# Performance work log

Measured on AMD Instinct MI355X. Metric: run time of the kernel, lower is better.

The kernel has to match this reference:

```python
import jax, jax.numpy as jnp
import numpy as np

B, H, KVH, D = 32, 32, 8, 128          # batch, q heads, kv heads, head_size
S = 2048                                # context length per sequence
BLOCK_SIZE = 16                         # tokens per cache block
NUM_BLOCKS = B * (S // BLOCK_SIZE)      # 4096
BASE = 10000.0
SCALE = 1.0 / D ** 0.5


def setup_inputs() -> dict:
    key = jax.random.key(0)
    kq, kk, kv = jax.random.split(key, 3)
    query = jax.random.normal(kq, (B, H, D), dtype=jnp.float32)
    # paged KV cache: [num_blocks, block_size * kv_heads * head_size]
    k_cache = jax.random.normal(kk, (NUM_BLOCKS, BLOCK_SIZE * KVH * D), dtype=jnp.float32)
    v_cache = jax.random.normal(kv, (NUM_BLOCKS, BLOCK_SIZE * KVH * D), dtype=jnp.float32)
    # contiguous slot layout: slot[i, p] = i * S + p  (>=0 means valid)
    slot_mapping = jnp.arange(B * S, dtype=jnp.int32).reshape(B, S)
    # per-sequence token positions 0..S-1
    positions = jnp.broadcast_to(jnp.arange(S, dtype=jnp.int32), (B, S))
    return {"query": query, "k_cache": k_cache, "v_cache": v_cache,
            "slot_mapping": slot_mapping, "positions": positions}


def _rope(x, pos):
    """x: [B, h, s, D], pos: [B, s] int -> rotary-embedded x (RotaryEmbedding.forward)."""
    inv_freq = 1.0 / (BASE ** (jnp.arange(0, D, 2, dtype=jnp.float32) / D))   # [D/2]
    freqs = pos[..., None].astype(jnp.float32) * inv_freq                     # [B, s, D/2]
    emb = jnp.concatenate([freqs, freqs], axis=-1)                            # [B, s, D]
    cos = jnp.cos(emb)[:, None]                                               # [B, 1, s, D]
    sin = jnp.sin(emb)[:, None]
    x1, x2 = x[..., : D // 2], x[..., D // 2 :]
    rotated = jnp.concatenate([-x2, x1], axis=-1)
    return x * cos + rotated * sin


def reference(query, k_cache, v_cache, slot_mapping, positions):
    # --- paged gather (the per-slot loop in _compatible_forward, vectorized) ---
    valid = slot_mapping >= 0                                  # [B, S]
    slots = jnp.where(valid, slot_mapping, 0)
    blk = slots // BLOCK_SIZE
    off = slots % BLOCK_SIZE
    kc = k_cache.reshape(NUM_BLOCKS, BLOCK_SIZE, KVH, D)
    vc = v_cache.reshape(NUM_BLOCKS, BLOCK_SIZE, KVH, D)
    k = kc[blk, off]                                           # [B, S, KVH, D]
    v = vc[blk, off]
    m = valid[..., None, None]
    k = jnp.where(m, k, 0.0).transpose(0, 2, 1, 3)             # [B, KVH, S, D]
    v = jnp.where(m, v, 0.0).transpose(0, 2, 1, 3)

    # --- rotary: q at its (last) position, keys at all cached positions ---
    q = query[:, :, None, :]                                   # [B, H, 1, D]
    q = _rope(q, positions[:, -1:])
    k = _rope(k, positions)

    # --- GQA: repeat_interleave kv heads to match q heads ---
    rep = H // KVH
    k = jnp.repeat(k, rep, axis=1)                             # [B, H, S, D]
    v = jnp.repeat(v, rep, axis=1)

    scores = jnp.einsum('bhqd,bhkd->bhqk', q, k) * SCALE       # [B, H, 1, S]
    weights = jax.nn.softmax(scores, axis=-1)
    out = jnp.einsum('bhqk,bhkd->bhqd', weights, v)            # [B, H, 1, D]
    return out[:, :, 0, :]                                     # [B, H, D]
```

## Files before the change

kernel.cpp:

```cpp
#include <hip/hip_runtime.h>
#include <math.h>

#define B_    32
#define H_    32
#define KVH_  8
#define D_    128
#define S_    2048
#define REP   4
#define PAIRS 256
#define SCALE 0.08838834764831845f

typedef unsigned int u32;

__device__ __forceinline__ void dma16(const float* g, float* l) {
    __builtin_amdgcn_global_load_lds(
        (const __attribute__((address_space(1))) u32*)g,
        (__attribute__((address_space(3))) u32*)l,
        16, 0, 0);
}

#define WAITVM(N) asm volatile("s_waitcnt vmcnt(" #N ")" ::: "memory")

__global__ __launch_bounds__(64) void rope_q(
    const float* __restrict__ query,
    const int*   __restrict__ positions,
    float* __restrict__ q_rot,
    float* __restrict__ invf_tab)
{
    const int head = blockIdx.x;
    const int b    = head >> 5;
    const int j    = threadIdx.x;
    const double invf = exp(-(double)j * (9.210340371976184 / 64.0));
    if (head == 0) invf_tab[j] = (float)invf;
    const int posq = positions[b * S_ + (S_ - 1)];
    const double fr = (double)posq * invf;
    const float cs = (float)cos(fr), sn = (float)sin(fr);
    const float* q = query + (size_t)head * D_;
    const float lo = q[j], hi = q[64 + j];
    float* o = q_rot + (size_t)head * D_;
    o[j]      = (lo * cs - hi * sn) * SCALE;
    o[64 + j] = (hi * cs + lo * sn) * SCALE;
}

extern __shared__ char smem_raw[];

__global__ __launch_bounds__(128, 4) void pa_main(
    const float* __restrict__ query,
    const float* __restrict__ k_cache,
    const float* __restrict__ v_cache,
    const int*   __restrict__ slot_map,
    const int*   __restrict__ positions,
    const float* __restrict__ q_rot,
    const float* __restrict__ invf_tab,
    float* __restrict__ ws_l,
    float* __restrict__ ws_acc,
    float* __restrict__ out,
    int cpp, int wpb, int use_qrot)
{
    const int w     = threadIdx.x >> 6;
    const int ln    = threadIdx.x & 63;
    const int g     = ln & 15;
    const int ts    = ln >> 4;
    const int chunk = S_ / cpp;
    const int gch   = blockIdx.x * wpb + w;
    const int pair  = gch / cpp;
    const int c     = gch - pair * cpp;
    const int b     = pair >> 3;
    const int kvh   = pair & 7;
    const int t0    = c * chunk;
    const int bS    = b * S_;
    const int passes = chunk >> 2;

    char*  wbase = smem_raw + (size_t)w * (8192 + 8 * chunk);
    float* buf   = (float*)wbase;
    int*   ls    = (int*)(wbase + 8192);
    int*   lp    = ls + chunk;

    for (int t = ln; t < chunk; t += 64) {
        ls[t] = slot_map[bS + t0 + t];
        lp[t] = positions[bS + t0 + t];
    }

    float ql[4][4], qh[4][4], invf[4];
    if (use_qrot) {
        float4 iv = ((const float4*)invf_tab)[g];
        invf[0] = iv.x; invf[1] = iv.y; invf[2] = iv.z; invf[3] = iv.w;
        #pragma unroll
        for (int hh = 0; hh < REP; hh++) {
            const float4* qb = (const float4*)(q_rot + (size_t)(b * H_ + kvh * REP + hh) * D_);
            float4 a = qb[g], cc = qb[16 + g];
            ql[hh][0] = a.x;  ql[hh][1] = a.y;  ql[hh][2] = a.z;  ql[hh][3] = a.w;
            qh[hh][0] = cc.x; qh[hh][1] = cc.y; qh[hh][2] = cc.z; qh[hh][3] = cc.w;
        }
    } else {
        #pragma unroll
        for (int j = 0; j < 4; j++)
            invf[j] = (float)exp(-(double)(4 * g + j) * (9.210340371976184 / 64.0));
        const int posq = positions[bS + (S_ - 1)];
        #pragma unroll
        for (int hh = 0; hh < REP; hh++) {
            const float4* qb = (const float4*)(query + (size_t)(b * H_ + kvh * REP + hh) * D_);
            float4 a = qb[g], cc = qb[16 + g];
            float al[4] = {a.x, a.y, a.z, a.w};
            float ah[4] = {cc.x, cc.y, cc.z, cc.w};
            #pragma unroll
            for (int j = 0; j < 4; j++) {
                double fr = (double)posq * exp(-(double)(4 * g + j) * (9.210340371976184 / 64.0));
                float cs = (float)cos(fr), sn = (float)sin(fr);
                ql[hh][j] = (al[j] * cs - ah[j] * sn) * SCALE;
                qh[hh][j] = (ah[j] * cs + al[j] * sn) * SCALE;
            }
        }
    }

    float acc_lo[4][4] = {};
    float acc_hi[4][4] = {};
    float lsum[4] = {0.f, 0.f, 0.f, 0.f};

    auto issue = [&](int pi, int bi) {
        const int tix = pi * 4 + ts;
        const int sl  = ls[tix];
        const int sc  = sl < 0 ? 0 : sl;
        const int ro  = (sc >> 4) * 16384 + (sc & 15) * 1024 + kvh * 128 + 4 * g;
        const float* kr = k_cache + ro;
        const float* vr = v_cache + ro;
        float* bp = buf + bi * 1024;
        dma16(kr,      bp);
        dma16(kr + 64, bp + 256);
        dma16(vr,      bp + 512);
        dma16(vr + 64, bp + 768);
    };

    issue(0, 0);
    for (int i = 0; i < passes; ++i) {
        const int ni = (i + 1 < passes) ? i + 1 : i;
        issue(ni, (i + 1) & 1);

        WAITVM(4);
        __builtin_amdgcn_sched_barrier(0);

        const float4* bf4 = (const float4*)(buf + (i & 1) * 1024);
        float4 k1 = bf4[ln];
        float4 k2 = bf4[64 + ln];

        const int tix = i * 4 + ts;
        const int sl  = ls[tix];
        const float m  = (sl >= 0) ? 1.f : 0.f;
        const float pf = (float)lp[tix];

        float kl[4], kh[4];
        {
            float kx[4] = {k1.x, k1.y, k1.z, k1.w};
            float ky[4] = {k2.x, k2.y, k2.z, k2.w};
            #pragma unroll
            for (int j = 0; j < 4; j++) {
                float fr = pf * invf[j];
                float sn, cs;
                __sincosf(fr, &sn, &cs);
                kl[j] = (kx[j] * cs - ky[j] * sn) * m;
                kh[j] = (ky[j] * cs + kx[j] * sn) * m;
            }
        }

        float p[4];
        #pragma unroll
        for (int hh = 0; hh < 4; hh++) {
            float t = ql[hh][0] * kl[0];
            t += ql[hh][1] * kl[1];
            t += ql[hh][2] * kl[2];
            t += ql[hh][3] * kl[3];
            t += qh[hh][0] * kh[0];
            t += qh[hh][1] * kh[1];
            t += qh[hh][2] * kh[2];
            t += qh[hh][3] * kh[3];
            p[hh] = t;
        }
        #pragma unroll
        for (int hh = 0; hh < 4; hh++) {
            #pragma unroll
            for (int mm = 1; mm < 16; mm <<= 1)
                p[hh] += __shfl_xor(p[hh], mm);
        }

        float4 v1 = bf4[128 + ln];
        float4 v2 = bf4[192 + ln];
        float vx[4] = {v1.x * m, v1.y * m, v1.z * m, v1.w * m};
        float vy[4] = {v2.x * m, v2.y * m, v2.z * m, v2.w * m};

        #pragma unroll
        for (int hh = 0; hh < 4; hh++) {
            const float wgt = __expf(p[hh]);
            lsum[hh] += wgt;
            #pragma unroll
            for (int j = 0; j < 4; j++) {
                acc_lo[hh][j] += wgt * vx[j];
                acc_hi[hh][j] += wgt * vy[j];
            }
        }
    }
    WAITVM(0);

    #pragma unroll
    for (int hh = 0; hh < 4; hh++) {
        lsum[hh] += __shfl_xor(lsum[hh], 16);
        lsum[hh] += __shfl_xor(lsum[hh], 32);
        #pragma unroll
        for (int j = 0; j < 4; j++) {
            acc_lo[hh][j] += __shfl_xor(acc_lo[hh][j], 16);
            acc_lo[hh][j] += __shfl_xor(acc_lo[hh][j], 32);
            acc_hi[hh][j] += __shfl_xor(acc_hi[hh][j], 16);
            acc_hi[hh][j] += __shfl_xor(acc_hi[hh][j], 32);
        }
    }

    if (cpp > 1) {
        if (ln < 16) {
            const size_t base = (size_t)(pair * cpp + c) * 4;
            #pragma unroll
            for (int hh = 0; hh < 4; hh++) {
                float4* dst = (float4*)(ws_acc + (base + hh) * 128);
                dst[g]      = make_float4(acc_lo[hh][0], acc_lo[hh][1], acc_lo[hh][2], acc_lo[hh][3]);
                dst[16 + g] = make_float4(acc_hi[hh][0], acc_hi[hh][1], acc_hi[hh][2], acc_hi[hh][3]);
            }
            if (ln == 0)
                *(float4*)(ws_l + base) = make_float4(lsum[0], lsum[1], lsum[2], lsum[3]);
        }
    } else {
        if (ln < 16) {
            #pragma unroll
            for (int hh = 0; hh < 4; hh++) {
                const float r = 1.f / lsum[hh];
                float4* dst = (float4*)(out + (size_t)(b * H_ + kvh * REP + hh) * D_);
                dst[g]      = make_float4(acc_lo[hh][0] * r, acc_lo[hh][1] * r, acc_lo[hh][2] * r, acc_lo[hh][3] * r);
                dst[16 + g] = make_float4(acc_hi[hh][0] * r, acc_hi[hh][1] * r, acc_hi[hh][2] * r, acc_hi[hh][3] * r);
            }
        }
    }
}

__global__ __launch_bounds__(512) void pa_reduce(
    const float* __restrict__ ws_l,
    const float* __restrict__ ws_acc,
    float* __restrict__ out,
    int cpp)
{
    const int pair = blockIdx.x;
    const int b = pair >> 3, kvh = pair & 7;
    const int hh = threadIdx.x >> 7;
    const int d  = threadIdx.x & 127;
    float a = 0.f;
    for (int s = 0; s < cpp; s++)
        a += ws_acc[((size_t)(pair * cpp + s) * 4 + hh) * 128 + d];
    float lt = 0.f;
    for (int s = 0; s < cpp; s++)
        lt += ws_l[(pair * cpp + s) * 4 + hh];
    out[((size_t)(b * H_ + kvh * REP + hh)) * D_ + d] = a / lt;
}

extern "C" void kernel_launch(void* const* d_in, const int* in_sizes, int n_in,
                              void* d_out, int out_size, void* d_ws, size_t ws_size,
                              hipStream_t stream) {
    const float* query = (const float*)d_in[0];
    const float* kc    = (const float*)d_in[1];
    const float* vc    = (const float*)d_in[2];
    const int*   sm    = (const int*)d_in[3];
    const int*   pos   = (const int*)d_in[4];
    float* out = (float*)d_out;

    const size_t qrot_f = (size_t)B_ * H_ * D_ + 64;
    int cpp = 1;
    int use_qrot = 0;
    const int cands[5] = {32, 16, 8, 4, 2};
    for (int ci = 0; ci < 5; ci++) {
        size_t need = (qrot_f + (size_t)PAIRS * cands[ci] * 516) * sizeof(float);
        if (ws_size >= need) { cpp = cands[ci]; use_qrot = 1; break; }
    }
    if (cpp == 1 && ws_size >= qrot_f * sizeof(float)) use_qrot = 1;

    float* q_rot    = (float*)d_ws;
    float* invf_tab = q_rot + (size_t)B_ * H_ * D_;
    float* ws_l     = use_qrot ? (invf_tab + 64) : (float*)d_ws;
    float* ws_acc   = ws_l + (size_t)PAIRS * cpp * 4;

    if (use_qrot)
        rope_q<<<dim3(B_ * H_), dim3(64), 0, stream>>>(query, pos, q_rot, invf_tab);

    const int wpb   = (cpp >= 2) ? 2 : 1;
    const int chunk = S_ / cpp;
    const size_t dynlds = (size_t)wpb * (8192 + 8 * chunk);
    pa_main<<<dim3(PAIRS * cpp / wpb), dim3(64 * wpb), dynlds, stream>>>(
        query, kc, vc, sm, pos, q_rot, invf_tab, ws_l, ws_acc, out, cpp, wpb, use_qrot);
    if (cpp > 1)
        pa_reduce<<<dim3(PAIRS), dim3(512), 0, stream>>>(ws_l, ws_acc, out, cpp);
}
```

Before: 552.8 us.

## Replace LDS DMA double buffer with register-based 4-deep prefetch

Drops the global_load_lds double-buffered staging and instead loads K/V rows straight into registers, prefetching four passes ahead in a register ring. This removes the LDS round trip and explicit vmcnt waits and raises the number of loads in flight, at the cost of more VGPRs. It also removes the occupancy hint from launch bounds and shrinks dynamic LDS to just the slot and position tables.

```diff
diff --git a/kernel.cpp b/kernel.cpp
--- a/kernel.cpp
+++ b/kernel.cpp
@@ -9,17 +9,6 @@
 #define REP   4
 #define PAIRS 256
 #define SCALE 0.08838834764831845f
-
-typedef unsigned int u32;
-
-__device__ __forceinline__ void dma16(const float* g, float* l) {
-    __builtin_amdgcn_global_load_lds(
-        (const __attribute__((address_space(1))) u32*)g,
-        (__attribute__((address_space(3))) u32*)l,
-        16, 0, 0);
-}
-
-#define WAITVM(N) asm volatile("s_waitcnt vmcnt(" #N ")" ::: "memory")
 
 __global__ __launch_bounds__(64) void rope_q(
     const float* __restrict__ query,
@@ -44,7 +33,7 @@
 
 extern __shared__ char smem_raw[];
 
-__global__ __launch_bounds__(128, 4) void pa_main(
+__global__ __launch_bounds__(128) void pa_main(
     const float* __restrict__ query,
     const float* __restrict__ k_cache,
     const float* __restrict__ v_cache,
@@ -71,10 +60,8 @@
     const int bS    = b * S_;
     const int passes = chunk >> 2;
 
-    char*  wbase = smem_raw + (size_t)w * (8192 + 8 * chunk);
-    float* buf   = (float*)wbase;
-    int*   ls    = (int*)(wbase + 8192);
-    int*   lp    = ls + chunk;
+    int* ls = (int*)(smem_raw + (size_t)w * (8 * chunk));
+    int* lp = ls + chunk;
 
     for (int t = ln; t < chunk; t += 64) {
         ls[t] = slot_map[bS + t0 + t];
@@ -117,32 +104,20 @@
     float acc_hi[4][4] = {};
     float lsum[4] = {0.f, 0.f, 0.f, 0.f};
 
-    auto issue = [&](int pi, int bi) {
+    float4 kb[4][2], vb[4][2];
+
+    auto ldpass = [&](int pi, int s) {
         const int tix = pi * 4 + ts;
         const int sl  = ls[tix];
         const int sc  = sl < 0 ? 0 : sl;
-        const int ro  = (sc >> 4) * 16384 + (sc & 15) * 1024 + kvh * 128 + 4 * g;
-        const float* kr = k_cache + ro;
-        const float* vr = v_cache + ro;
-        float* bp = buf + bi * 1024;
-        dma16(kr,      bp);
-        dma16(kr + 64, bp + 256);
-        dma16(vr,      bp + 512);
-        dma16(vr + 64, bp + 768);
+        const size_t ro = (size_t)(sc >> 4) * 16384 + (size_t)(sc & 15) * 1024 + kvh * 128 + 4 * g;
+        const float4* kr = (const float4*)(k_cache + ro);
+        const float4* vr = (const float4*)(v_cache + ro);
+        kb[s][0] = kr[0];  kb[s][1] = kr[16];
+        vb[s][0] = vr[0];  vb[s][1] = vr[16];
     };
 
-    issue(0, 0);
-    for (int i = 0; i < passes; ++i) {
-        const int ni = (i + 1 < passes) ? i + 1 : i;
-        issue(ni, (i + 1) & 1);
-
-        WAITVM(4);
-        __builtin_amdgcn_sched_barrier(0);
-
-        const float4* bf4 = (const float4*)(buf + (i & 1) * 1024);
-        float4 k1 = bf4[ln];
-        float4 k2 = bf4[64 + ln];
-
+    auto compute = [&](int i, int s) {
         const int tix = i * 4 + ts;
         const int sl  = ls[tix];
         const float m  = (sl >= 0) ? 1.f : 0.f;
@@ -150,8 +125,8 @@
 
         float kl[4], kh[4];
         {
-            float kx[4] = {k1.x, k1.y, k1.z, k1.w};
-            float ky[4] = {k2.x, k2.y, k2.z, k2.w};
+            float kx[4] = {kb[s][0].x, kb[s][0].y, kb[s][0].z, kb[s][0].w};
+            float ky[4] = {kb[s][1].x, kb[s][1].y, kb[s][1].z, kb[s][1].w};
             #pragma unroll
             for (int j = 0; j < 4; j++) {
                 float fr = pf * invf[j];
@@ -182,10 +157,8 @@
                 p[hh] += __shfl_xor(p[hh], mm);
         }
 
-        float4 v1 = bf4[128 + ln];
-        float4 v2 = bf4[192 + ln];
-        float vx[4] = {v1.x * m, v1.y * m, v1.z * m, v1.w * m};
-        float vy[4] = {v2.x * m, v2.y * m, v2.z * m, v2.w * m};
+        float vx[4] = {vb[s][0].x * m, vb[s][0].y * m, vb[s][0].z * m, vb[s][0].w * m};
+        float vy[4] = {vb[s][1].x * m, vb[s][1].y * m, vb[s][1].z * m, vb[s][1].w * m};
 
         #pragma unroll
         for (int hh = 0; hh < 4; hh++) {
@@ -197,8 +170,21 @@
                 acc_hi[hh][j] += wgt * vy[j];
             }
         }
-    }
-    WAITVM(0);
+    };
+
+    #pragma unroll
+    for (int j = 0; j < 4; ++j)
+        ldpass(j, j);
+
+    for (int base = 0; base < passes; base += 4) {
+        #pragma unroll
+        for (int j = 0; j < 4; ++j) {
+            const int i = base + j;
+            compute(i, j);
+            if (i + 4 < passes)
+                ldpass(i + 4, j);
+        }
+    }
 
     #pragma unroll
     for (int hh = 0; hh < 4; hh++) {
@@ -287,7 +273,7 @@
 
     const int wpb   = (cpp >= 2) ? 2 : 1;
     const int chunk = S_ / cpp;
-    const size_t dynlds = (size_t)wpb * (8192 + 8 * chunk);
+    const size_t dynlds = (size_t)wpb * (8 * chunk);
     pa_main<<<dim3(PAIRS * cpp / wpb), dim3(64 * wpb), dynlds, stream>>>(
         query, kc, vc, sm, pos, q_rot, invf_tab, ws_l, ws_acc, out, cpp, wpb, use_qrot);
     if (cpp > 1)
```

Measured after the change: 534.0 us. 1.04x faster.
